# Kernel tuning notes

Hardware: AMD Instinct MI355X
Metric: run time of the kernel (lower is better)

The kernel has to match this reference:

```python
import jax, jax.numpy as jnp
import numpy as np

BS, IN_SIZE, OUT_SIZE, FEATS = 32, 1024, 1024, 2048


def setup_inputs() -> dict:
    key = jax.random.key(0)
    kx, kw = jax.random.split(key)
    x = jax.random.normal(kx, (BS, IN_SIZE, FEATS), dtype=jnp.float32)
    # Per-sample weight matrices (the stacked nn.Parameters, kernel-size-1 conv
    # weights of shape [out_size, in_size, 1] -> squeezed to [out_size, in_size]).
    weights = jax.random.normal(kw, (BS, OUT_SIZE, IN_SIZE), dtype=jnp.float32)
    return {"x": x, "weights": weights}


def reference(x, weights):
    # F.conv2d(x.view(1, bs*in_size, feats), W.view(bs*out_size, in_size, 1), groups=bs)
    # with kernel size 1 is exactly a per-sample matmul:
    # out[b, o, f] = sum_i weights[b, o, i] * x[b, i, f]
    return jnp.einsum('boi,bif->bof', weights, x)
```

## Files before the change

### kernel.cpp

```cpp
#include <hip/hip_runtime.h>
#include <hip/hip_bf16.h>
#include <string.h>


typedef float  f32x2 __attribute__((ext_vector_type(2)));
typedef float  f32x4 __attribute__((ext_vector_type(4)));
typedef short  bf16x8 __attribute__((ext_vector_type(8)));
typedef unsigned int u32;

#define BATCH 32
#define MDIM 1024
#define KDIM 1024
#define NDIM 2048
#define BM 256
#define BN 256
#define BK 32
#define NT (KDIM / BK)
#define LSTR 36

__device__ __forceinline__ u32 cvt2(float a, float b) {
    float2 t; t.x = a; t.y = b;
    __hip_bfloat162 h = __float22bfloat162_rn(t);
    u32 r; memcpy(&r, &h, 4);
    return r;
}

__device__ __forceinline__ void lds_barrier() {
    asm volatile("s_waitcnt lgkmcnt(0)" ::: "memory");
    __builtin_amdgcn_s_barrier();
    asm volatile("" ::: "memory");
}

__global__ __launch_bounds__(512, 2) void bgemm_bf16_kernel(
    const float* __restrict__ x, const float* __restrict__ w,
    float* __restrict__ out)
{
    __shared__ unsigned short Ab[2][BM * LSTR];
    __shared__ unsigned short Bb[2][BN * LSTR];

    const int bid  = blockIdx.x;
    const int lbid = (bid & 7) * 128 + (bid >> 3);
    const int bx = lbid & 7;
    const int by = (lbid >> 3) & 3;
    const int bz = lbid >> 5;

    const int tid = threadIdx.x;
    const int m0  = by * BM;
    const int n0  = bx * BN;

    const int lane = tid & 63;
    const int wid  = tid >> 6;
    const int wm   = (wid >> 2) * 128;
    const int wn   = (wid & 3)  * 64;
    const int l15  = lane & 15;
    const int kg8  = (lane >> 4) * 8;

    const float* Ag = w + (size_t)bz * MDIM * KDIM + (size_t)m0 * KDIM;
    const float* Bg = x + (size_t)bz * KDIM * NDIM + n0;
    float*       Cg = out + (size_t)bz * MDIM * NDIM + (size_t)m0 * NDIM + n0;

    const int a_k4 = tid & 7;
    const int a_m0 = tid >> 3;
    int a_idx[4];
    #pragma unroll
    for (int i = 0; i < 4; ++i)
        a_idx[i] = (a_m0 + 64 * i) * LSTR + 4 * a_k4;
    const int bn0  = 2 * (tid & 127);
    const int b_k0 = 8 * (tid >> 7);
    int b_idx[2];
    #pragma unroll
    for (int c = 0; c < 2; ++c)
        b_idx[c] = (bn0 + c) * LSTR + b_k0;
    int rd_a[8], rd_b[4];
    #pragma unroll
    for (int mi = 0; mi < 8; ++mi)
        rd_a[mi] = (wm + mi * 16 + l15) * LSTR + kg8;
    #pragma unroll
    for (int ni = 0; ni < 4; ++ni)
        rd_b[ni] = (wn + ni * 16 + l15) * LSTR + kg8;

    const float* Ap = Ag + (size_t)a_m0 * KDIM + 4 * a_k4;
    const float* Bp = Bg + (size_t)b_k0 * NDIM + bn0;

    f32x4 acc[8][4];
    #pragma unroll
    for (int i = 0; i < 8; ++i)
        #pragma unroll
        for (int j = 0; j < 4; ++j)
            acc[i][j] = f32x4{0.f, 0.f, 0.f, 0.f};

    f32x4 aav[4];
    f32x2 bbv[8];

    auto load_regs = [&](int kt) {
        #pragma unroll
        for (int i = 0; i < 4; ++i)
            aav[i] = *reinterpret_cast<const f32x4*>(Ap + (size_t)(64 * i) * KDIM + kt);
        #pragma unroll
        for (int j = 0; j < 8; ++j)
            bbv[j] = *reinterpret_cast<const f32x2*>(Bp + (size_t)(kt + j) * NDIM);
    };
    auto stage = [&](int s) {
        #pragma unroll
        for (int i = 0; i < 4; ++i) {
            uint2 v = make_uint2(cvt2(aav[i][0], aav[i][1]),
                                 cvt2(aav[i][2], aav[i][3]));
            *reinterpret_cast<uint2*>(&Ab[s][a_idx[i]]) = v;
        }
        #pragma unroll
        for (int c = 0; c < 2; ++c) {
            uint4 v = make_uint4(cvt2(bbv[0][c], bbv[1][c]),
                                 cvt2(bbv[2][c], bbv[3][c]),
                                 cvt2(bbv[4][c], bbv[5][c]),
                                 cvt2(bbv[6][c], bbv[7][c]));
            *reinterpret_cast<uint4*>(&Bb[s][b_idx[c]]) = v;
        }
    };
    auto compute = [&](int s) {
        bf16x8 bfr[4];
        #pragma unroll
        for (int ni = 0; ni < 4; ++ni)
            bfr[ni] = *reinterpret_cast<const bf16x8*>(&Bb[s][rd_b[ni]]);
        #pragma unroll
        for (int mi = 0; mi < 8; ++mi) {
            bf16x8 af = *reinterpret_cast<const bf16x8*>(&Ab[s][rd_a[mi]]);
            #pragma unroll
            for (int ni = 0; ni < 4; ++ni)
                acc[mi][ni] = __builtin_amdgcn_mfma_f32_16x16x32_bf16(
                    af, bfr[ni], acc[mi][ni], 0, 0, 0);
        }
    };

    load_regs(0);
    stage(0);
    load_regs(BK);
    lds_barrier();

    for (int t = 0; t < NT - 1; ++t) {
        const int cur = t & 1;
        stage(cur ^ 1);
        int kt2 = (t + 2) * BK;
        if (kt2 > KDIM - BK) kt2 = KDIM - BK;
        load_regs(kt2);
        compute(cur);
        lds_barrier();
    }
    compute((NT - 1) & 1);

    const int rbase = (lane >> 4) * 4;
    #pragma unroll
    for (int mi = 0; mi < 8; ++mi) {
        #pragma unroll
        for (int ni = 0; ni < 4; ++ni) {
            int n  = wn + ni * 16 + l15;
            int mb = wm + mi * 16 + rbase;
            #pragma unroll
            for (int r = 0; r < 4; ++r)
                Cg[(size_t)(mb + r) * NDIM + n] = acc[mi][ni][r];
        }
    }
}

extern "C" void kernel_launch(void* const* d_in, const int* in_sizes, int n_in,
                              void* d_out, int out_size, void* d_ws, size_t ws_size,
                              hipStream_t stream) {
    const float* x = (const float*)d_in[0];
    const float* w = (const float*)d_in[1];
    float* out = (float*)d_out;
    const int nblocks = (NDIM / BN) * (MDIM / BM) * BATCH;
    bgemm_bf16_kernel<<<dim3(nblocks), dim3(512), 0, stream>>>(x, w, out);
}
```

Measured before the change: 243.5 us.

## Split MFMA block into halves interleaved with staging and global loads

The per-iteration compute is split into two halves of 16 MFMAs. LDS fragment reads for the current buffer are issued first, then the bf16 staging writes and the next global loads are placed between the two MFMA halves. Each MFMA half is wrapped in s_setprio raises so that matrix work gets issue priority across waves. The aim is to hide LDS, conversion and global-load latency behind matrix instructions. The cost is more live registers at 2 waves/SIMD occupancy, which could cause spills.

```diff
diff --git a/kernel.cpp b/kernel.cpp
--- a/kernel.cpp
+++ b/kernel.cpp
@@ -116,20 +116,6 @@
             *reinterpret_cast<uint4*>(&Bb[s][b_idx[c]]) = v;
         }
     };
-    auto compute = [&](int s) {
-        bf16x8 bfr[4];
-        #pragma unroll
-        for (int ni = 0; ni < 4; ++ni)
-            bfr[ni] = *reinterpret_cast<const bf16x8*>(&Bb[s][rd_b[ni]]);
-        #pragma unroll
-        for (int mi = 0; mi < 8; ++mi) {
-            bf16x8 af = *reinterpret_cast<const bf16x8*>(&Ab[s][rd_a[mi]]);
-            #pragma unroll
-            for (int ni = 0; ni < 4; ++ni)
-                acc[mi][ni] = __builtin_amdgcn_mfma_f32_16x16x32_bf16(
-                    af, bfr[ni], acc[mi][ni], 0, 0, 0);
-        }
-    };
 
     load_regs(0);
     stage(0);
@@ -138,14 +124,61 @@
 
     for (int t = 0; t < NT - 1; ++t) {
         const int cur = t & 1;
+        bf16x8 bfr[4], af1[4];
+
+        #pragma unroll
+        for (int ni = 0; ni < 4; ++ni)
+            bfr[ni] = *reinterpret_cast<const bf16x8*>(&Bb[cur][rd_b[ni]]);
+        #pragma unroll
+        for (int mi = 0; mi < 4; ++mi)
+            af1[mi] = *reinterpret_cast<const bf16x8*>(&Ab[cur][rd_a[mi]]);
+
         stage(cur ^ 1);
+
+        __builtin_amdgcn_s_setprio(1);
+        #pragma unroll
+        for (int mi = 0; mi < 4; ++mi)
+            #pragma unroll
+            for (int ni = 0; ni < 4; ++ni)
+                acc[mi][ni] = __builtin_amdgcn_mfma_f32_16x16x32_bf16(
+                    af1[mi], bfr[ni], acc[mi][ni], 0, 0, 0);
+        __builtin_amdgcn_s_setprio(0);
+
+        bf16x8 af2[4];
+        #pragma unroll
+        for (int mi = 0; mi < 4; ++mi)
+            af2[mi] = *reinterpret_cast<const bf16x8*>(&Ab[cur][rd_a[mi + 4]]);
         int kt2 = (t + 2) * BK;
         if (kt2 > KDIM - BK) kt2 = KDIM - BK;
         load_regs(kt2);
-        compute(cur);
+
+        __builtin_amdgcn_s_setprio(1);
+        #pragma unroll
+        for (int mi = 0; mi < 4; ++mi)
+            #pragma unroll
+            for (int ni = 0; ni < 4; ++ni)
+                acc[mi + 4][ni] = __builtin_amdgcn_mfma_f32_16x16x32_bf16(
+                    af2[mi], bfr[ni], acc[mi + 4][ni], 0, 0, 0);
+        __builtin_amdgcn_s_setprio(0);
+
         lds_barrier();
     }
-    compute((NT - 1) & 1);
+
+    {
+        const int cur = (NT - 1) & 1;
+        bf16x8 bfr[4];
+        #pragma unroll
+        for (int ni = 0; ni < 4; ++ni)
+            bfr[ni] = *reinterpret_cast<const bf16x8*>(&Bb[cur][rd_b[ni]]);
+        #pragma unroll
+        for (int mi = 0; mi < 8; ++mi) {
+            bf16x8 af = *reinterpret_cast<const bf16x8*>(&Ab[cur][rd_a[mi]]);
+            #pragma unroll
+            for (int ni = 0; ni < 4; ++ni)
+                acc[mi][ni] = __builtin_amdgcn_mfma_f32_16x16x32_bf16(
+                    af, bfr[ni], acc[mi][ni], 0, 0, 0);
+        }
+    }
 
     const int rbase = (lane >> 4) * 4;
     #pragma unroll
```

After: 250.8 us. +3.0%, slower.

## Split block into producer and consumer warps for load and MFMA

Applied to the files above, without the earlier changes.

Restructures the batched GEMM so that 4 producer waves load fp32 tiles, convert them to bf16 and stage them into double-buffered LDS, while 8 consumer waves only run MFMAs on 64x128 sub-tiles. Block size grows to 768 threads with launch bounds targeting 3 blocks per CU, and the LDS row stride changes from 36 to 34. The aim is to overlap global-load and convert latency with tensor-core work through warp specialization. In exchange, each producer thread now holds twice as many load registers, and with only two LDS buffers the two roles still meet at a barrier every k-step, so overlap is limited and occupancy or register pressure may suffer.

```diff
diff --git a/kernel.cpp b/kernel.cpp
--- a/kernel.cpp
+++ b/kernel.cpp
@@ -3,7 +3,6 @@
 #include <string.h>
 
 
-typedef float  f32x2 __attribute__((ext_vector_type(2)));
 typedef float  f32x4 __attribute__((ext_vector_type(4)));
 typedef short  bf16x8 __attribute__((ext_vector_type(8)));
 typedef unsigned int u32;
@@ -16,7 +15,7 @@
 #define BN 256
 #define BK 32
 #define NT (KDIM / BK)
-#define LSTR 36
+#define LSTR 34
 
 __device__ __forceinline__ u32 cvt2(float a, float b) {
     float2 t; t.x = a; t.y = b;
@@ -31,7 +30,7 @@
     asm volatile("" ::: "memory");
 }
 
-__global__ __launch_bounds__(512, 2) void bgemm_bf16_kernel(
+__global__ __launch_bounds__(768, 3) void bgemm_pc_kernel(
     const float* __restrict__ x, const float* __restrict__ w,
     float* __restrict__ out)
 {
@@ -44,119 +43,121 @@
     const int by = (lbid >> 3) & 3;
     const int bz = lbid >> 5;
 
-    const int tid = threadIdx.x;
-    const int m0  = by * BM;
-    const int n0  = bx * BN;
+    const int tid  = threadIdx.x;
+    const int wid  = tid >> 6;
+    const int lane = tid & 63;
 
-    const int lane = tid & 63;
-    const int wid  = tid >> 6;
-    const int wm   = (wid >> 2) * 128;
-    const int wn   = (wid & 3)  * 64;
-    const int l15  = lane & 15;
-    const int kg8  = (lane >> 4) * 8;
+    const float* Ag = w + (size_t)bz * MDIM * KDIM + (size_t)(by * BM) * KDIM;
+    const float* Bg = x + (size_t)bz * KDIM * NDIM + bx * BN;
 
-    const float* Ag = w + (size_t)bz * MDIM * KDIM + (size_t)m0 * KDIM;
-    const float* Bg = x + (size_t)bz * KDIM * NDIM + n0;
-    float*       Cg = out + (size_t)bz * MDIM * NDIM + (size_t)m0 * NDIM + n0;
+    if (wid < 4) {
+        const int a_k4 = tid & 7;
+        const int a_m0 = tid >> 3;
+        int a_idx[8];
+        #pragma unroll
+        for (int i = 0; i < 8; ++i)
+            a_idx[i] = (a_m0 + 32 * i) * LSTR + 4 * a_k4;
+        const int bn0  = 4 * (tid & 63);
+        const int b_k0 = 8 * (tid >> 6);
+        int b_idx[4];
+        #pragma unroll
+        for (int c = 0; c < 4; ++c)
+            b_idx[c] = (bn0 + c) * LSTR + b_k0;
 
-    const int a_k4 = tid & 7;
-    const int a_m0 = tid >> 3;
-    int a_idx[4];
-    #pragma unroll
-    for (int i = 0; i < 4; ++i)
-        a_idx[i] = (a_m0 + 64 * i) * LSTR + 4 * a_k4;
-    const int bn0  = 2 * (tid & 127);
-    const int b_k0 = 8 * (tid >> 7);
-    int b_idx[2];
-    #pragma unroll
-    for (int c = 0; c < 2; ++c)
-        b_idx[c] = (bn0 + c) * LSTR + b_k0;
-    int rd_a[8], rd_b[4];
-    #pragma unroll
-    for (int mi = 0; mi < 8; ++mi)
-        rd_a[mi] = (wm + mi * 16 + l15) * LSTR + kg8;
-    #pragma unroll
-    for (int ni = 0; ni < 4; ++ni)
-        rd_b[ni] = (wn + ni * 16 + l15) * LSTR + kg8;
+        const float* Ap = Ag + (size_t)a_m0 * KDIM + 4 * a_k4;
+        const float* Bp = Bg + (size_t)b_k0 * NDIM + bn0;
 
-    const float* Ap = Ag + (size_t)a_m0 * KDIM + 4 * a_k4;
-    const float* Bp = Bg + (size_t)b_k0 * NDIM + bn0;
+        f32x4 aav[8], bbv[8];
+        auto load_regs = [&](int kt) {
+            #pragma unroll
+            for (int i = 0; i < 8; ++i)
+                aav[i] = *reinterpret_cast<const f32x4*>(
+                    Ap + (size_t)(32 * i) * KDIM + kt);
+            #pragma unroll
+            for (int j = 0; j < 8; ++j)
+                bbv[j] = *reinterpret_cast<const f32x4*>(
+                    Bp + (size_t)(kt + j) * NDIM);
+        };
+        auto stage = [&](int s) {
+            #pragma unroll
+            for (int i = 0; i < 8; ++i) {
+                uint2 v = make_uint2(cvt2(aav[i][0], aav[i][1]),
+                                     cvt2(aav[i][2], aav[i][3]));
+                *reinterpret_cast<uint2*>(&Ab[s][a_idx[i]]) = v;
+            }
+            #pragma unroll
+            for (int c = 0; c < 4; ++c) {
+                uint4 v = make_uint4(cvt2(bbv[0][c], bbv[1][c]),
+                                     cvt2(bbv[2][c], bbv[3][c]),
+                                     cvt2(bbv[4][c], bbv[5][c]),
+                                     cvt2(bbv[6][c], bbv[7][c]));
+                *reinterpret_cast<uint4*>(&Bb[s][b_idx[c]]) = v;
+            }
+        };
 
-    f32x4 acc[8][4];
-    #pragma unroll
-    for (int i = 0; i < 8; ++i)
+        load_regs(0);
+        stage(0);
+        load_regs(BK);
+        lds_barrier();
+        for (int t = 1; t < NT; ++t) {
+            stage(t & 1);
+            if (t + 1 < NT)
+                load_regs((t + 1) * BK);
+            lds_barrier();
+        }
+    } else {
+        const int cw  = wid - 4;
+        const int wm  = (cw >> 1) * 64;
+        const int wn  = (cw & 1) * 128;
+        const int l15 = lane & 15;
+        const int kg8 = (lane >> 4) * 8;
+
+        int rd_a[4], rd_b[8];
         #pragma unroll
-        for (int j = 0; j < 4; ++j)
-            acc[i][j] = f32x4{0.f, 0.f, 0.f, 0.f};
+        for (int mi = 0; mi < 4; ++mi)
+            rd_a[mi] = (wm + mi * 16 + l15) * LSTR + kg8;
+        #pragma unroll
+        for (int ni = 0; ni < 8; ++ni)
+            rd_b[ni] = (wn + ni * 16 + l15) * LSTR + kg8;
 
-    f32x4 aav[4];
-    f32x2 bbv[8];
-
-    auto load_regs = [&](int kt) {
+        f32x4 acc[4][8];
         #pragma unroll
         for (int i = 0; i < 4; ++i)
-            aav[i] = *reinterpret_cast<const f32x4*>(Ap + (size_t)(64 * i) * KDIM + kt);
+            #pragma unroll
+            for (int j = 0; j < 8; ++j)
+                acc[i][j] = f32x4{0.f, 0.f, 0.f, 0.f};
+
+        lds_barrier();
+        for (int t = 0; t < NT; ++t) {
+            const int s = t & 1;
+            bf16x8 af[4];
+            #pragma unroll
+            for (int mi = 0; mi < 4; ++mi)
+                af[mi] = *reinterpret_cast<const bf16x8*>(&Ab[s][rd_a[mi]]);
+            #pragma unroll
+            for (int ni = 0; ni < 8; ++ni) {
+                bf16x8 bfr = *reinterpret_cast<const bf16x8*>(&Bb[s][rd_b[ni]]);
+                #pragma unroll
+                for (int mi = 0; mi < 4; ++mi)
+                    acc[mi][ni] = __builtin_amdgcn_mfma_f32_16x16x32_bf16(
+                        af[mi], bfr, acc[mi][ni], 0, 0, 0);
+            }
+            if (t < NT - 1) lds_barrier();
+        }
+
+        float* Cg = out + (size_t)bz * MDIM * NDIM
+                        + (size_t)(by * BM) * NDIM + bx * BN;
+        const int rbase = (lane >> 4) * 4;
         #pragma unroll
-        for (int j = 0; j < 8; ++j)
-            bbv[j] = *reinterpret_cast<const f32x2*>(Bp + (size_t)(kt + j) * NDIM);
-    };
-    auto stage = [&](int s) {
-        #pragma unroll
-        for (int i = 0; i < 4; ++i) {
-            uint2 v = make_uint2(cvt2(aav[i][0], aav[i][1]),
-                                 cvt2(aav[i][2], aav[i][3]));
-            *reinterpret_cast<uint2*>(&Ab[s][a_idx[i]]) = v;
-        }
-        #pragma unroll
-        for (int c = 0; c < 2; ++c) {
-            uint4 v = make_uint4(cvt2(bbv[0][c], bbv[1][c]),
-                                 cvt2(bbv[2][c], bbv[3][c]),
-                                 cvt2(bbv[4][c], bbv[5][c]),
-                                 cvt2(bbv[6][c], bbv[7][c]));
-            *reinterpret_cast<uint4*>(&Bb[s][b_idx[c]]) = v;
-        }
-    };
-    auto compute = [&](int s) {
-        bf16x8 bfr[4];
-        #pragma unroll
-        for (int ni = 0; ni < 4; ++ni)
-            bfr[ni] = *reinterpret_cast<const bf16x8*>(&Bb[s][rd_b[ni]]);
-        #pragma unroll
-        for (int mi = 0; mi < 8; ++mi) {
-            bf16x8 af = *reinterpret_cast<const bf16x8*>(&Ab[s][rd_a[mi]]);
+        for (int mi = 0; mi < 4; ++mi) {
             #pragma unroll
-            for (int ni = 0; ni < 4; ++ni)
-                acc[mi][ni] = __builtin_amdgcn_mfma_f32_16x16x32_bf16(
-                    af, bfr[ni], acc[mi][ni], 0, 0, 0);
-        }
-    };
-
-    load_regs(0);
-    stage(0);
-    load_regs(BK);
-    lds_barrier();
-
-    for (int t = 0; t < NT - 1; ++t) {
-        const int cur = t & 1;
-        stage(cur ^ 1);
-        int kt2 = (t + 2) * BK;
-        if (kt2 > KDIM - BK) kt2 = KDIM - BK;
-        load_regs(kt2);
-        compute(cur);
-        lds_barrier();
-    }
-    compute((NT - 1) & 1);
-
-    const int rbase = (lane >> 4) * 4;
-    #pragma unroll
-    for (int mi = 0; mi < 8; ++mi) {
-        #pragma unroll
-        for (int ni = 0; ni < 4; ++ni) {
-            int n  = wn + ni * 16 + l15;
-            int mb = wm + mi * 16 + rbase;
-            #pragma unroll
-            for (int r = 0; r < 4; ++r)
-                Cg[(size_t)(mb + r) * NDIM + n] = acc[mi][ni][r];
+            for (int ni = 0; ni < 8; ++ni) {
+                int n  = wn + ni * 16 + l15;
+                int mb = wm + mi * 16 + rbase;
+                #pragma unroll
+                for (int r = 0; r < 4; ++r)
+                    Cg[(size_t)(mb + r) * NDIM + n] = acc[mi][ni][r];
+            }
         }
     }
 }
@@ -168,5 +169,5 @@
     const float* w = (const float*)d_in[1];
     float* out = (float*)d_out;
     const int nblocks = (NDIM / BN) * (MDIM / BM) * BATCH;
-    bgemm_bf16_kernel<<<dim3(nblocks), dim3(512), 0, stream>>>(x, w, out);
+    bgemm_pc_kernel<<<dim3(nblocks), dim3(768), 0, stream>>>(x, w, out);
 }
```

Measured after the change: 259.3 us. 6.5% more time.

## Switch to 32x32x16 MFMA, BK=64, and interleave staging with compute quarters

Applied to the files above, without the earlier changes.

Replaces the 16x16x32 bf16 MFMA tiles with 32x32x16 tiles, which halves the number of LDS fragment reads per FLOP. It doubles the K tile to 64 so there are half as many barriers. Global loads and LDS staging for the next tile are split into halves and interleaved between four compute quarters, and the MFMA bursts run at raised wave priority (s_setprio). The larger LDS buffers (two 256x68 bf16 tiles per operand, double-buffered) may limit occupancy at two blocks per CU. Register pressure also goes up.

```diff
diff --git a/kernel.cpp b/kernel.cpp
--- a/kernel.cpp
+++ b/kernel.cpp
@@ -5,6 +5,7 @@
 
 typedef float  f32x2 __attribute__((ext_vector_type(2)));
 typedef float  f32x4 __attribute__((ext_vector_type(4)));
+typedef float  f32x16 __attribute__((ext_vector_type(16)));
 typedef short  bf16x8 __attribute__((ext_vector_type(8)));
 typedef unsigned int u32;
 
@@ -14,9 +15,9 @@
 #define NDIM 2048
 #define BM 256
 #define BN 256
-#define BK 32
+#define BK 64
 #define NT (KDIM / BK)
-#define LSTR 36
+#define LSTR 68
 
 __device__ __forceinline__ u32 cvt2(float a, float b) {
     float2 t; t.x = a; t.y = b;
@@ -44,68 +45,66 @@
     const int by = (lbid >> 3) & 3;
     const int bz = lbid >> 5;
 
-    const int tid = threadIdx.x;
-    const int m0  = by * BM;
-    const int n0  = bx * BN;
-
+    const int tid  = threadIdx.x;
     const int lane = tid & 63;
     const int wid  = tid >> 6;
     const int wm   = (wid >> 2) * 128;
     const int wn   = (wid & 3)  * 64;
-    const int l15  = lane & 15;
-    const int kg8  = (lane >> 4) * 8;
+    const int l31  = lane & 31;
+    const int kg8  = (lane >> 5) * 8;
 
-    const float* Ag = w + (size_t)bz * MDIM * KDIM + (size_t)m0 * KDIM;
-    const float* Bg = x + (size_t)bz * KDIM * NDIM + n0;
-    float*       Cg = out + (size_t)bz * MDIM * NDIM + (size_t)m0 * NDIM + n0;
+    const float* Ag = w + (size_t)bz * MDIM * KDIM + (size_t)(by * BM) * KDIM;
+    const float* Bg = x + (size_t)bz * KDIM * NDIM + bx * BN;
+    float*       Cg = out + (size_t)bz * MDIM * NDIM
+                          + (size_t)(by * BM) * NDIM + bx * BN;
 
-    const int a_k4 = tid & 7;
-    const int a_m0 = tid >> 3;
-    int a_idx[4];
+    const int a_k4 = tid & 15;
+    const int a_m0 = tid >> 4;
+    int a_idx[8];
     #pragma unroll
-    for (int i = 0; i < 4; ++i)
-        a_idx[i] = (a_m0 + 64 * i) * LSTR + 4 * a_k4;
+    for (int i = 0; i < 8; ++i)
+        a_idx[i] = (a_m0 + 32 * i) * LSTR + 4 * a_k4;
     const int bn0  = 2 * (tid & 127);
     const int b_k0 = 8 * (tid >> 7);
     int b_idx[2];
     #pragma unroll
     for (int c = 0; c < 2; ++c)
         b_idx[c] = (bn0 + c) * LSTR + b_k0;
-    int rd_a[8], rd_b[4];
+    int rd_a[4], rd_b[2];
     #pragma unroll
-    for (int mi = 0; mi < 8; ++mi)
-        rd_a[mi] = (wm + mi * 16 + l15) * LSTR + kg8;
+    for (int fm = 0; fm < 4; ++fm)
+        rd_a[fm] = (wm + fm * 32 + l31) * LSTR + kg8;
     #pragma unroll
-    for (int ni = 0; ni < 4; ++ni)
-        rd_b[ni] = (wn + ni * 16 + l15) * LSTR + kg8;
+    for (int fn = 0; fn < 2; ++fn)
+        rd_b[fn] = (wn + fn * 32 + l31) * LSTR + kg8;
 
     const float* Ap = Ag + (size_t)a_m0 * KDIM + 4 * a_k4;
     const float* Bp = Bg + (size_t)b_k0 * NDIM + bn0;
 
-    f32x4 acc[8][4];
+    f32x16 acc[8];
     #pragma unroll
     for (int i = 0; i < 8; ++i)
-        #pragma unroll
-        for (int j = 0; j < 4; ++j)
-            acc[i][j] = f32x4{0.f, 0.f, 0.f, 0.f};
+        acc[i] = (f32x16)(0.f);
 
     f32x4 aav[4];
     f32x2 bbv[8];
 
-    auto load_regs = [&](int kt) {
+    auto load_regs = [&](int kt, int h) {
         #pragma unroll
         for (int i = 0; i < 4; ++i)
-            aav[i] = *reinterpret_cast<const f32x4*>(Ap + (size_t)(64 * i) * KDIM + kt);
+            aav[i] = *reinterpret_cast<const f32x4*>(
+                Ap + (size_t)(32 * (i + 4 * h)) * KDIM + kt);
         #pragma unroll
         for (int j = 0; j < 8; ++j)
-            bbv[j] = *reinterpret_cast<const f32x2*>(Bp + (size_t)(kt + j) * NDIM);
+            bbv[j] = *reinterpret_cast<const f32x2*>(
+                Bp + (size_t)(kt + 32 * h + j) * NDIM);
     };
-    auto stage = [&](int s) {
+    auto stage = [&](int s, int h) {
         #pragma unroll
         for (int i = 0; i < 4; ++i) {
             uint2 v = make_uint2(cvt2(aav[i][0], aav[i][1]),
                                  cvt2(aav[i][2], aav[i][3]));
-            *reinterpret_cast<uint2*>(&Ab[s][a_idx[i]]) = v;
+            *reinterpret_cast<uint2*>(&Ab[s][a_idx[i + 4 * h]]) = v;
         }
         #pragma unroll
         for (int c = 0; c < 2; ++c) {
@@ -113,50 +112,72 @@
                                  cvt2(bbv[2][c], bbv[3][c]),
                                  cvt2(bbv[4][c], bbv[5][c]),
                                  cvt2(bbv[6][c], bbv[7][c]));
-            *reinterpret_cast<uint4*>(&Bb[s][b_idx[c]]) = v;
+            *reinterpret_cast<uint4*>(&Bb[s][b_idx[c] + 32 * h]) = v;
         }
     };
-    auto compute = [&](int s) {
-        bf16x8 bfr[4];
+    auto quarter = [&](int s, int ks) {
+        bf16x8 af[4], bf[2];
+        const int ko = 16 * ks;
         #pragma unroll
-        for (int ni = 0; ni < 4; ++ni)
-            bfr[ni] = *reinterpret_cast<const bf16x8*>(&Bb[s][rd_b[ni]]);
+        for (int fn = 0; fn < 2; ++fn)
+            bf[fn] = *reinterpret_cast<const bf16x8*>(&Bb[s][rd_b[fn] + ko]);
         #pragma unroll
-        for (int mi = 0; mi < 8; ++mi) {
-            bf16x8 af = *reinterpret_cast<const bf16x8*>(&Ab[s][rd_a[mi]]);
+        for (int fm = 0; fm < 4; ++fm)
+            af[fm] = *reinterpret_cast<const bf16x8*>(&Ab[s][rd_a[fm] + ko]);
+        __builtin_amdgcn_s_setprio(1);
+        #pragma unroll
+        for (int fm = 0; fm < 4; ++fm)
             #pragma unroll
-            for (int ni = 0; ni < 4; ++ni)
-                acc[mi][ni] = __builtin_amdgcn_mfma_f32_16x16x32_bf16(
-                    af, bfr[ni], acc[mi][ni], 0, 0, 0);
-        }
+            for (int fn = 0; fn < 2; ++fn)
+                acc[fm * 2 + fn] = __builtin_amdgcn_mfma_f32_32x32x16_bf16(
+                    af[fm], bf[fn], acc[fm * 2 + fn], 0, 0, 0);
+        __builtin_amdgcn_s_setprio(0);
     };
 
-    load_regs(0);
-    stage(0);
-    load_regs(BK);
+    load_regs(0, 0);
+    stage(0, 0);
+    load_regs(0, 1);
+    stage(0, 1);
+    load_regs(BK, 0);
     lds_barrier();
 
     for (int t = 0; t < NT - 1; ++t) {
         const int cur = t & 1;
-        stage(cur ^ 1);
+        const int ktn = (t + 1) * BK;
+
+        quarter(cur, 0);
+        stage(cur ^ 1, 0);
+        load_regs(ktn, 1);
+        quarter(cur, 1);
+        quarter(cur, 2);
+        stage(cur ^ 1, 1);
         int kt2 = (t + 2) * BK;
         if (kt2 > KDIM - BK) kt2 = KDIM - BK;
-        load_regs(kt2);
-        compute(cur);
+        load_regs(kt2, 0);
+        quarter(cur, 3);
+
         lds_barrier();
     }
-    compute((NT - 1) & 1);
 
-    const int rbase = (lane >> 4) * 4;
+    {
+        const int cur = (NT - 1) & 1;
+        #pragma unroll
+        for (int ks = 0; ks < 4; ++ks)
+            quarter(cur, ks);
+    }
+
+    const int rbase = 4 * (lane >> 5);
     #pragma unroll
-    for (int mi = 0; mi < 8; ++mi) {
+    for (int fm = 0; fm < 4; ++fm) {
         #pragma unroll
-        for (int ni = 0; ni < 4; ++ni) {
-            int n  = wn + ni * 16 + l15;
-            int mb = wm + mi * 16 + rbase;
+        for (int fn = 0; fn < 2; ++fn) {
+            const f32x16& a16 = acc[fm * 2 + fn];
+            const int n = wn + fn * 32 + l31;
             #pragma unroll
-            for (int r = 0; r < 4; ++r)
-                Cg[(size_t)(mb + r) * NDIM + n] = acc[mi][ni][r];
+            for (int r = 0; r < 16; ++r) {
+                int row = wm + fm * 32 + (r & 3) + 8 * (r >> 2) + rbase;
+                Cg[(size_t)row * NDIM + n] = a16[r];
+            }
         }
     }
 }
```

Measured after the change: 250.6 us. 1.03x slower.
